# Kernel optimization log

Measured on AMD Instinct MI355X. Metric: run time of the kernel, lower is better.

Reference implementation:

```python
import jax, jax.numpy as jnp
import numpy as np

B, S, D, H = 2, 2048, 1024, 16
DK = D // H

def setup_inputs() -> dict:
    key = jax.random.key(0)
    ks = jax.random.split(key, 12)
    s = 1.0 / np.sqrt(D)
    return {
        "q": jax.random.normal(ks[0], (B, S, D), jnp.float32),
        "k": jax.random.normal(ks[1], (B, S, D), jnp.float32),
        "v": jax.random.normal(ks[2], (B, S, D), jnp.float32),
        "mask": jnp.ones((1, 1, S, S), jnp.int32),
        "Wq": jax.random.normal(ks[3], (D, D), jnp.float32) * s,
        "bq": jnp.zeros((D,), jnp.float32),
        "Wk": jax.random.normal(ks[4], (D, D), jnp.float32) * s,
        "bk": jnp.zeros((D,), jnp.float32),
        "Wv": jax.random.normal(ks[5], (D, D), jnp.float32) * s,
        "bv": jnp.zeros((D,), jnp.float32),
        "Wo": jax.random.normal(ks[6], (D, D), jnp.float32) * s,
        "bo": jnp.zeros((D,), jnp.float32),
    }

def reference(q, k, v, mask, Wq, bq, Wk, bk, Wv, bv, Wo, bo):
    # projections (torch Linear: x @ W^T + b)
    Q = q @ Wq.T + bq
    K = k @ Wk.T + bk
    V = v @ Wv.T + bv
    # split heads: [B,S,D] -> [B,H,S,DK]
    def split(x):
        return x.reshape(B, S, H, DK).transpose(0, 2, 1, 3)
    Qh, Kh, Vh = split(Q), split(K), split(V)
    scores = jnp.einsum('bhqd,bhkd->bhqk', Qh, Kh) / jnp.sqrt(jnp.float32(DK))
    scores = jnp.where(mask == 0, jnp.float32(-1e9), scores)
    attn = jax.nn.softmax(scores, axis=-1)  # dropout p=0.0 -> identity
    x = jnp.einsum('bhqk,bhkd->bhqd', attn, Vh)
    x = x.transpose(0, 2, 1, 3).reshape(B, S, D)
    return x @ Wo.T + bo
```

## Files before the change

kernel.cpp:

```cpp
#include <hip/hip_runtime.h>
#include <hip/hip_bf16.h>
#include <stdint.h>

#define B_    2
#define S_    2048
#define D_    1024
#define H_    16
#define NTOK  (B_ * S_)

typedef __attribute__((ext_vector_type(8))) short bf16x8;
typedef __attribute__((ext_vector_type(4))) float f32x4;
typedef __attribute__((ext_vector_type(2))) float float2v;
typedef __attribute__((ext_vector_type(2))) __bf16 bfv2;

static __device__ __forceinline__ unsigned int pkbf(float a, float b) {
    float2v fv = {a, b};
    bfv2 r = __builtin_convertvector(fv, bfv2);
    unsigned int u;
    __builtin_memcpy(&u, &r, 4);
    return u;
}

using g_cu32 = __attribute__((address_space(1))) const unsigned int;
using l_u32  = __attribute__((address_space(3))) unsigned int;
static __device__ __forceinline__ void gld16(const void* g, void* l) {
    __builtin_amdgcn_global_load_lds((g_cu32*)g, (l_u32*)l, 16, 0, 0);
}

#define QN ((size_t)NTOK * D_)
#define WN ((size_t)D_ * D_)

struct SwapT { static constexpr bool value = true; };
struct NoSwapT { static constexpr bool value = false; };

__global__ __launch_bounds__(256) void prep_kernel(
    const float* __restrict__ q, const float* __restrict__ k, const float* __restrict__ v,
    const float* __restrict__ Wq, const float* __restrict__ Wk,
    const float* __restrict__ Wv, const float* __restrict__ Wo,
    const int* __restrict__ mask,
    unsigned short* __restrict__ qb, unsigned short* __restrict__ kb,
    unsigned short* __restrict__ vb, unsigned short* __restrict__ wqb,
    unsigned short* __restrict__ wkb, unsigned short* __restrict__ wvb,
    unsigned short* __restrict__ wob, int* __restrict__ flags) {
    __shared__ int anyz;
    if (blockIdx.x < 8192) {
        size_t i = ((size_t)blockIdx.x * 256 + threadIdx.x) * 8;
        const float* s; unsigned short* d; size_t off;
        if (i < QN)          { s = q; d = qb; off = i; }
        else if (i < 2 * QN) { s = k; d = kb; off = i - QN; }
        else if (i < 3 * QN) { s = v; d = vb; off = i - 2 * QN; }
        else {
            size_t j = i - 3 * QN;
            int wi = (int)(j >> 20);
            s = (wi == 0) ? Wq : (wi == 1) ? Wk : (wi == 2) ? Wv : Wo;
            d = (wi == 0) ? wqb : (wi == 1) ? wkb : (wi == 2) ? wvb : wob;
            off = j & (WN - 1);
        }
        float4 a = *(const float4*)(s + off);
        float4 b = *(const float4*)(s + off + 4);
        uint4 pk;
        pk.x = pkbf(a.x, a.y); pk.y = pkbf(a.z, a.w);
        pk.z = pkbf(b.x, b.y); pk.w = pkbf(b.z, b.w);
        *(uint4*)(d + off) = pk;
    } else {
        if (threadIdx.x == 0) anyz = 0;
        __syncthreads();
        int bid2 = blockIdx.x - 8192;
        const int qt = bid2 >> 5, kt = bid2 & 31;
        int az = 0;
        for (int i = threadIdx.x; i < 64 * 64; i += 256) {
            int r = i >> 6, c = i & 63;
            az |= (mask[(size_t)(qt * 64 + r) * S_ + kt * 64 + c] == 0) ? 1 : 0;
        }
        if (az) atomicOr(&anyz, 1);
        __syncthreads();
        if (threadIdx.x == 0) flags[qt * 32 + kt] = anyz;
    }
}

struct GemmArgs {
    const unsigned short* A[3];
    const unsigned short* W[3];
    const float* bias[3];
    void* C[3];
    int mode[3];
    float scale[3];
};

template<int BMT>
__global__ __launch_bounds__(256, 3) void gemm_async(GemmArgs ga) {
    constexpr int AG = BMT / 16;
    constexpr int MI = BMT / 32;
    constexpr int NK = D_ / 32;
    const int z = blockIdx.z;
    const unsigned short* __restrict__ A = ga.A[z];
    const unsigned short* __restrict__ W = ga.W[z];
    const float* __restrict__ bias = ga.bias[z];
    void* C = ga.C[z];
    const int mode = ga.mode[z];
    const float scl = ga.scale[z];

    __shared__ unsigned short As[2][AG * 512];
    __shared__ unsigned short Bs[2][8 * 512];

    const int t    = threadIdx.x;
    const int lane = t & 63;
    const int w    = t >> 6;
    const int fr   = lane & 15;
    const int kq   = lane >> 4;
    const int wrow = w >> 1, wcol = w & 1;
    const int m0 = blockIdx.x * BMT, n0 = blockIdx.y * 128;

    const int sc = lane >> 4;
    const int sr = lane & 15;

    const unsigned short* ga0;
    const unsigned short* ga1 = nullptr;
    int la0Off, la1Off = 0;
    if constexpr (BMT == 128) {
        ga0 = A + (size_t)(m0 + (2 * w) * 16 + sr) * D_ + sc * 8;
        ga1 = ga0 + 16 * D_;
        la0Off = (2 * w) * 512;
        la1Off = (2 * w + 1) * 512;
    } else {
        ga0 = A + (size_t)(m0 + w * 16 + sr) * D_ + sc * 8;
        la0Off = w * 512;
    }
    const unsigned short* gw0 = W + (size_t)(n0 + (2 * w) * 16 + sr) * D_ + sc * 8;
    const unsigned short* gw1 = gw0 + 16 * D_;
    const int lw0Off = (2 * w) * 512;
    const int lw1Off = (2 * w + 1) * 512;

    int aOff[MI], bOff[4];
#pragma unroll
    for (int mi = 0; mi < MI; ++mi) aOff[mi] = (wrow * MI + mi) * 512 + (kq * 16 + fr) * 8;
#pragma unroll
    for (int ni = 0; ni < 4; ++ni) bOff[ni] = (wcol * 4 + ni) * 512 + (kq * 16 + fr) * 8;

    f32x4 acc[MI][4];
#pragma unroll
    for (int i = 0; i < MI; ++i)
#pragma unroll
        for (int j = 0; j < 4; ++j) acc[i][j] = (f32x4)0.0f;

    auto stage = [&](int buf) {
        gld16(ga0, &As[buf][la0Off]);
        if constexpr (BMT == 128) gld16(ga1, &As[buf][la1Off]);
        gld16(gw0, &Bs[buf][lw0Off]);
        gld16(gw1, &Bs[buf][lw1Off]);
        ga0 += 32; gw0 += 32; gw1 += 32;
        if constexpr (BMT == 128) ga1 += 32;
    };

    auto kloop = [&](auto swc) {
        constexpr bool SW = decltype(swc)::value;
        stage(0);
        for (int k0 = 0; k0 < NK; ++k0) {
            const int cur = k0 & 1;
            __syncthreads();
            if (k0 < NK - 1) stage(cur ^ 1);

            bf16x8 af[MI], bfr[4];
#pragma unroll
            for (int mi = 0; mi < MI; ++mi) af[mi] = *(const bf16x8*)&As[cur][aOff[mi]];
#pragma unroll
            for (int ni = 0; ni < 4; ++ni) bfr[ni] = *(const bf16x8*)&Bs[cur][bOff[ni]];
#pragma unroll
            for (int mi = 0; mi < MI; ++mi)
#pragma unroll
                for (int ni = 0; ni < 4; ++ni) {
                    if constexpr (SW)
                        acc[mi][ni] = __builtin_amdgcn_mfma_f32_16x16x32_bf16(
                            bfr[ni], af[mi], acc[mi][ni], 0, 0, 0);
                    else
                        acc[mi][ni] = __builtin_amdgcn_mfma_f32_16x16x32_bf16(
                            af[mi], bfr[ni], acc[mi][ni], 0, 0, 0);
                }
        }
    };
    if (mode == 2) kloop(NoSwapT{}); else kloop(SwapT{});

    if (mode == 2) {
        unsigned short* Co = (unsigned short*)C;
#pragma unroll
        for (int ni = 0; ni < 4; ++ni) {
            int col = n0 + wcol * 64 + ni * 16 + fr;
            float bv = bias[col];
            int hh = col >> 6, d = col & 63;
#pragma unroll
            for (int mi = 0; mi < MI; ++mi) {
                int tok = m0 + wrow * (BMT / 2) + mi * 16 + kq * 4;
                int bb = tok >> 11, sbase = tok & (S_ - 1);
                uint2 pk;
                pk.x = pkbf((acc[mi][ni][0] + bv) * scl, (acc[mi][ni][1] + bv) * scl);
                pk.y = pkbf((acc[mi][ni][2] + bv) * scl, (acc[mi][ni][3] + bv) * scl);
                *(uint2*)(Co + ((size_t)((bb * H_ + hh) * 64 + d)) * S_ + sbase) = pk;
            }
        }
    } else if (mode == 0) {
        float* Co = (float*)C;
#pragma unroll
        for (int ni = 0; ni < 4; ++ni) {
            int nb = n0 + wcol * 64 + ni * 16 + kq * 4;
            float4 b4 = *(const float4*)&bias[nb];
#pragma unroll
            for (int mi = 0; mi < MI; ++mi) {
                int m = m0 + wrow * (BMT / 2) + mi * 16 + fr;
                float4 o4;
                o4.x = (acc[mi][ni][0] + b4.x) * scl;
                o4.y = (acc[mi][ni][1] + b4.y) * scl;
                o4.z = (acc[mi][ni][2] + b4.z) * scl;
                o4.w = (acc[mi][ni][3] + b4.w) * scl;
                *(float4*)(Co + (size_t)m * D_ + nb) = o4;
            }
        }
    } else {
        unsigned short* Co = (unsigned short*)C;
#pragma unroll
        for (int ni = 0; ni < 4; ++ni) {
            int nb = n0 + wcol * 64 + ni * 16 + kq * 4;
            float4 b4 = *(const float4*)&bias[nb];
#pragma unroll
            for (int mi = 0; mi < MI; ++mi) {
                int m = m0 + wrow * (BMT / 2) + mi * 16 + fr;
                uint2 pk;
                pk.x = pkbf((acc[mi][ni][0] + b4.x) * scl, (acc[mi][ni][1] + b4.y) * scl);
                pk.y = pkbf((acc[mi][ni][2] + b4.z) * scl, (acc[mi][ni][3] + b4.w) * scl);
                *(uint2*)(Co + (size_t)m * D_ + nb) = pk;
            }
        }
    }
}

__global__ __launch_bounds__(512, 4) void flash4(
    const unsigned short* __restrict__ Qb, const unsigned short* __restrict__ Kb,
    const unsigned short* __restrict__ Vtg, const int* __restrict__ mask,
    const int* __restrict__ flags, unsigned short* __restrict__ Xb) {
    __shared__ unsigned short Ks[2][4096];
    __shared__ unsigned short Vs[2][4096];
    __shared__ unsigned short Ps[8192];

    const int t    = threadIdx.x;
    const int lane = t & 63;
    const int w    = t >> 6;
    const int fr   = lane & 15;
    const int kq   = lane >> 4;
    const int bid = blockIdx.x;
    const int swb = ((bid & 7) << 6) | (bid >> 3);
    const int qt = swb & 15, hd = (swb >> 4) & 15, b = swb >> 8;
    const int q0 = qt * 128;
    const int swz = fr & 7;

    const unsigned short* qrow_p = Qb + (size_t)(b * S_ + q0 + w * 16 + fr) * D_ + hd * 64;
    bf16x8 qf[2];
    qf[0] = *(const bf16x8*)(qrow_p + kq * 8);
    qf[1] = *(const bf16x8*)(qrow_p + 32 + kq * 8);

    int fl = (lane < 32) ? flags[(qt * 2 + (w >> 2)) * 32 + lane] : 0;
    unsigned int fmask = (unsigned int)__ballot(fl != 0);

    const unsigned short* kptr =
        Kb + (size_t)(b * S_ + (w >> 1) * 16 + fr) * D_ + hd * 64 + (w & 1) * 32 + kq * 8;
    const unsigned short* vptr =
        Vtg + ((size_t)((b * H_ + hd) * 64 + (w >> 1) * 16 + fr)) * S_ + (w & 1) * 32 + kq * 8;

    gld16(kptr, (char*)&Ks[0][0] + w * 1024);
    gld16(vptr, (char*)&Vs[0][0] + w * 1024);
    const unsigned short* kpf = kptr + (size_t)64 * D_;
    const unsigned short* vpf = vptr + 64;

    unsigned short* pswr[4];
#pragma unroll
    for (int mi = 0; mi < 4; ++mi) {
        int chunk = mi * 2 + (kq >> 1);
        pswr[mi] = &Ps[(w * 16 + fr) * 64 + ((chunk ^ swz) << 3) + ((kq & 1) << 2)];
    }
    const unsigned short* psrd[2];
#pragma unroll
    for (int kk = 0; kk < 2; ++kk) {
        int c = kk * 4 + kq;
        psrd[kk] = &Ps[(w * 16 + fr) * 64 + ((c ^ swz) << 3)];
    }

    const f32x4 zf = (f32x4)0.0f;
    f32x4 o[4];
#pragma unroll
    for (int i = 0; i < 4; ++i) o[i] = zf;
    float2v l2 = {0.0f, 0.0f};

    for (int kt = 0; kt < 32; ++kt) {
        const int cur = kt & 1;
        __syncthreads();
        if (kt < 31) {
            gld16(kpf, (char*)&Ks[cur ^ 1][0] + w * 1024);
            gld16(vpf, (char*)&Vs[cur ^ 1][0] + w * 1024);
            kpf += (size_t)64 * D_;
            vpf += 64;
        }

        f32x4 st[4];
#pragma unroll
        for (int mi = 0; mi < 4; ++mi) {
            bf16x8 a = *(const bf16x8*)&Ks[cur][mi * 1024 + (kq * 16 + fr) * 8];
            st[mi] = __builtin_amdgcn_mfma_f32_16x16x32_bf16(a, qf[0], zf, 0, 0, 0);
        }
#pragma unroll
        for (int mi = 0; mi < 4; ++mi) {
            bf16x8 a = *(const bf16x8*)&Ks[cur][mi * 1024 + ((4 + kq) * 16 + fr) * 8];
            st[mi] = __builtin_amdgcn_mfma_f32_16x16x32_bf16(a, qf[1], st[mi], 0, 0, 0);
        }

        if ((fmask >> kt) & 1u) {
#pragma unroll
            for (int mi = 0; mi < 4; ++mi) {
                int4 mv = *(const int4*)&mask[(size_t)(q0 + w * 16 + fr) * S_ + kt * 64 + mi * 16 + kq * 4];
                if (mv.x == 0) st[mi][0] = -3e8f;
                if (mv.y == 0) st[mi][1] = -3e8f;
                if (mv.z == 0) st[mi][2] = -3e8f;
                if (mv.w == 0) st[mi][3] = -3e8f;
            }
        }

#pragma unroll
        for (int mi = 0; mi < 4; ++mi) {
            float e0 = __builtin_amdgcn_exp2f(st[mi][0]);
            float e1 = __builtin_amdgcn_exp2f(st[mi][1]);
            float e2 = __builtin_amdgcn_exp2f(st[mi][2]);
            float e3 = __builtin_amdgcn_exp2f(st[mi][3]);
            l2 += (float2v){e0, e1} + (float2v){e2, e3};
            uint2 pk;
            pk.x = pkbf(e0, e1);
            pk.y = pkbf(e2, e3);
            *(uint2*)pswr[mi] = pk;
        }

#pragma unroll
        for (int kk = 0; kk < 2; ++kk) {
            bf16x8 pb = *(const bf16x8*)psrd[kk];
#pragma unroll
            for (int mi = 0; mi < 4; ++mi) {
                bf16x8 a = *(const bf16x8*)&Vs[cur][mi * 1024 + ((kk * 4 + kq) * 16 + fr) * 8];
                o[mi] = __builtin_amdgcn_mfma_f32_16x16x32_bf16(a, pb, o[mi], 0, 0, 0);
            }
        }
    }

    float l_i = l2.x + l2.y;
    l_i += __shfl_xor(l_i, 16, 64);
    l_i += __shfl_xor(l_i, 32, 64);
    float rl = 1.0f / l_i;

#pragma unroll
    for (int mi = 0; mi < 4; ++mi) {
        uint2 pk;
        pk.x = pkbf(o[mi][0] * rl, o[mi][1] * rl);
        pk.y = pkbf(o[mi][2] * rl, o[mi][3] * rl);
        *(uint2*)(Xb + (size_t)(b * S_ + q0 + w * 16 + fr) * D_ + hd * 64 + mi * 16 + kq * 4) = pk;
    }
}

extern "C" void kernel_launch(void* const* d_in, const int* in_sizes, int n_in,
                              void* d_out, int out_size, void* d_ws, size_t ws_size,
                              hipStream_t stream) {
    const float* q    = (const float*)d_in[0];
    const float* k    = (const float*)d_in[1];
    const float* v    = (const float*)d_in[2];
    const int*   mask = (const int*)d_in[3];
    const float* Wq   = (const float*)d_in[4];
    const float* bq   = (const float*)d_in[5];
    const float* Wk   = (const float*)d_in[6];
    const float* bk   = (const float*)d_in[7];
    const float* Wv   = (const float*)d_in[8];
    const float* bv   = (const float*)d_in[9];
    const float* Wo   = (const float*)d_in[10];
    const float* bo   = (const float*)d_in[11];
    float* out = (float*)d_out;

    unsigned short* qb  = (unsigned short*)d_ws;
    unsigned short* kb  = qb + QN;
    unsigned short* vb  = kb + QN;
    unsigned short* Qf  = vb + QN;
    unsigned short* Kf  = Qf + QN;
    unsigned short* Vt  = Kf + QN;
    unsigned short* wqb = Vt + QN;
    unsigned short* wkb = wqb + WN;
    unsigned short* wvb = wkb + WN;
    unsigned short* wob = wvb + WN;
    int* flags = (int*)(wob + WN);

    const float SC = 0.18033688011112042f;

    prep_kernel<<<9216, 256, 0, stream>>>(q, k, v, Wq, Wk, Wv, Wo, mask,
                                          qb, kb, vb, wqb, wkb, wvb, wob, flags);

    GemmArgs g1;
    g1.A[0] = qb;  g1.W[0] = wqb; g1.bias[0] = bq; g1.C[0] = Qf; g1.mode[0] = 1; g1.scale[0] = SC;
    g1.A[1] = kb;  g1.W[1] = wkb; g1.bias[1] = bk; g1.C[1] = Kf; g1.mode[1] = 1; g1.scale[1] = 1.0f;
    g1.A[2] = vb;  g1.W[2] = wvb; g1.bias[2] = bv; g1.C[2] = Vt; g1.mode[2] = 2; g1.scale[2] = 1.0f;
    gemm_async<128><<<dim3(NTOK / 128, D_ / 128, 3), 256, 0, stream>>>(g1);

    flash4<<<dim3((S_ / 128) * H_ * B_, 1, 1), 512, 0, stream>>>(Qf, Kf, Vt, mask, flags, Qf);

    GemmArgs g2;
    g2.A[0] = Qf; g2.W[0] = wob; g2.bias[0] = bo; g2.C[0] = out; g2.mode[0] = 0; g2.scale[0] = 1.0f;
    g2.A[1] = g2.A[2] = nullptr; g2.W[1] = g2.W[2] = nullptr;
    g2.bias[1] = g2.bias[2] = nullptr; g2.C[1] = g2.C[2] = nullptr;
    g2.mode[1] = g2.mode[2] = 0; g2.scale[1] = g2.scale[2] = 1.0f;
    gemm_async<64><<<dim3(NTOK / 64, D_ / 128, 1), 256, 0, stream>>>(g2);
}
```

Baseline: 263.2 us.

## Triple-buffer GEMM and flash-attention loads with explicit vmcnt waits

Moves both the projection GEMM and the flash-attention K/V loop from double to triple-buffered LDS staging, keeping two tiles in flight. The loops replace __syncthreads with a partial s_waitcnt vmcnt plus a raw s_barrier fenced by sched_barriers, so the newest prefetch can stay outstanding while the current tile is computed. This is meant to hide global-to-LDS latency, at the cost of more LDS per block, which may lower occupancy. Correctness depends on the vmcnt counts matching the number of loads issued per stage.

```diff
diff --git a/kernel.cpp b/kernel.cpp
--- a/kernel.cpp
+++ b/kernel.cpp
@@ -25,6 +25,13 @@
 using l_u32  = __attribute__((address_space(3))) unsigned int;
 static __device__ __forceinline__ void gld16(const void* g, void* l) {
     __builtin_amdgcn_global_load_lds((g_cu32*)g, (l_u32*)l, 16, 0, 0);
+}
+
+template<int N> static __device__ __forceinline__ void wait_vm() {
+    if constexpr (N == 0)      asm volatile("s_waitcnt vmcnt(0)" ::: "memory");
+    else if constexpr (N == 2) asm volatile("s_waitcnt vmcnt(2)" ::: "memory");
+    else if constexpr (N == 3) asm volatile("s_waitcnt vmcnt(3)" ::: "memory");
+    else if constexpr (N == 4) asm volatile("s_waitcnt vmcnt(4)" ::: "memory");
 }
 
 #define QN ((size_t)NTOK * D_)
@@ -92,6 +99,7 @@
     constexpr int AG = BMT / 16;
     constexpr int MI = BMT / 32;
     constexpr int NK = D_ / 32;
+    constexpr int LOADS = (BMT == 128) ? 4 : 3;
     const int z = blockIdx.z;
     const unsigned short* __restrict__ A = ga.A[z];
     const unsigned short* __restrict__ W = ga.W[z];
@@ -100,8 +108,8 @@
     const int mode = ga.mode[z];
     const float scl = ga.scale[z];
 
-    __shared__ unsigned short As[2][AG * 512];
-    __shared__ unsigned short Bs[2][8 * 512];
+    __shared__ unsigned short As[3][AG * 512];
+    __shared__ unsigned short Bs[3][8 * 512];
 
     const int t    = threadIdx.x;
     const int lane = t & 63;
@@ -154,17 +162,14 @@
 
     auto kloop = [&](auto swc) {
         constexpr bool SW = decltype(swc)::value;
-        stage(0);
-        for (int k0 = 0; k0 < NK; ++k0) {
-            const int cur = k0 & 1;
-            __syncthreads();
-            if (k0 < NK - 1) stage(cur ^ 1);
-
+        auto mma_step = [&](int cur) {
+            const unsigned short* Ab = As[cur];
+            const unsigned short* Bb = Bs[cur];
             bf16x8 af[MI], bfr[4];
 #pragma unroll
-            for (int mi = 0; mi < MI; ++mi) af[mi] = *(const bf16x8*)&As[cur][aOff[mi]];
-#pragma unroll
-            for (int ni = 0; ni < 4; ++ni) bfr[ni] = *(const bf16x8*)&Bs[cur][bOff[ni]];
+            for (int mi = 0; mi < MI; ++mi) af[mi] = *(const bf16x8*)&Ab[aOff[mi]];
+#pragma unroll
+            for (int ni = 0; ni < 4; ++ni) bfr[ni] = *(const bf16x8*)&Bb[bOff[ni]];
 #pragma unroll
             for (int mi = 0; mi < MI; ++mi)
 #pragma unroll
@@ -176,7 +181,28 @@
                         acc[mi][ni] = __builtin_amdgcn_mfma_f32_16x16x32_bf16(
                             af[mi], bfr[ni], acc[mi][ni], 0, 0, 0);
                 }
-        }
+        };
+
+        stage(0);
+        stage(1);
+        int cur = 0;
+        for (int k0 = 0; k0 < NK - 1; ++k0) {
+            __builtin_amdgcn_sched_barrier(0);
+            wait_vm<LOADS>();
+            __builtin_amdgcn_s_barrier();
+            __builtin_amdgcn_sched_barrier(0);
+            if (k0 + 2 < NK) {
+                int pf = (cur >= 1) ? cur - 1 : cur + 2;
+                stage(pf);
+            }
+            mma_step(cur);
+            cur = (cur < 2) ? cur + 1 : 0;
+        }
+        __builtin_amdgcn_sched_barrier(0);
+        wait_vm<0>();
+        __builtin_amdgcn_s_barrier();
+        __builtin_amdgcn_sched_barrier(0);
+        mma_step(cur);
     };
     if (mode == 2) kloop(NoSwapT{}); else kloop(SwapT{});
 
@@ -236,8 +262,8 @@
     const unsigned short* __restrict__ Qb, const unsigned short* __restrict__ Kb,
     const unsigned short* __restrict__ Vtg, const int* __restrict__ mask,
     const int* __restrict__ flags, unsigned short* __restrict__ Xb) {
-    __shared__ unsigned short Ks[2][4096];
-    __shared__ unsigned short Vs[2][4096];
+    __shared__ unsigned short Ks[3][4096];
+    __shared__ unsigned short Vs[3][4096];
     __shared__ unsigned short Ps[8192];
 
     const int t    = threadIdx.x;
@@ -266,8 +292,10 @@
 
     gld16(kptr, (char*)&Ks[0][0] + w * 1024);
     gld16(vptr, (char*)&Vs[0][0] + w * 1024);
-    const unsigned short* kpf = kptr + (size_t)64 * D_;
-    const unsigned short* vpf = vptr + 64;
+    gld16(kptr + (size_t)64 * D_, (char*)&Ks[1][0] + w * 1024);
+    gld16(vptr + 64,              (char*)&Vs[1][0] + w * 1024);
+    const unsigned short* kpf = kptr + (size_t)128 * D_;
+    const unsigned short* vpf = vptr + 128;
 
     unsigned short* pswr[4];
 #pragma unroll
@@ -288,16 +316,7 @@
     for (int i = 0; i < 4; ++i) o[i] = zf;
     float2v l2 = {0.0f, 0.0f};
 
-    for (int kt = 0; kt < 32; ++kt) {
-        const int cur = kt & 1;
-        __syncthreads();
-        if (kt < 31) {
-            gld16(kpf, (char*)&Ks[cur ^ 1][0] + w * 1024);
-            gld16(vpf, (char*)&Vs[cur ^ 1][0] + w * 1024);
-            kpf += (size_t)64 * D_;
-            vpf += 64;
-        }
-
+    auto attn_step = [&](int cur, int kt) {
         f32x4 st[4];
 #pragma unroll
         for (int mi = 0; mi < 4; ++mi) {
@@ -343,7 +362,29 @@
                 o[mi] = __builtin_amdgcn_mfma_f32_16x16x32_bf16(a, pb, o[mi], 0, 0, 0);
             }
         }
-    }
+    };
+
+    int cur = 0;
+    for (int kt = 0; kt < 31; ++kt) {
+        __builtin_amdgcn_sched_barrier(0);
+        wait_vm<2>();
+        __builtin_amdgcn_s_barrier();
+        __builtin_amdgcn_sched_barrier(0);
+        if (kt < 30) {
+            int pf = (cur >= 1) ? cur - 1 : cur + 2;
+            gld16(kpf, (char*)&Ks[pf][0] + w * 1024);
+            gld16(vpf, (char*)&Vs[pf][0] + w * 1024);
+            kpf += (size_t)64 * D_;
+            vpf += 64;
+        }
+        attn_step(cur, kt);
+        cur = (cur < 2) ? cur + 1 : 0;
+    }
+    __builtin_amdgcn_sched_barrier(0);
+    wait_vm<0>();
+    __builtin_amdgcn_s_barrier();
+    __builtin_amdgcn_sched_barrier(0);
+    attn_step(cur, 31);
 
     float l_i = l2.x + l2.y;
     l_i += __shfl_xor(l_i, 16, 64);
```

Result: no change. 260.6 us (-1.0%).
